# Kernel tuning notes

Measured on AMD Instinct MI355X. Metric: run time of the kernel, lower is better.

## Reference

```python
import jax, jax.numpy as jnp
import numpy as np

FFT_LEN = 512
HOP_LEN = 256
N_BLOCK = 4
N_BIN = FFT_LEN // 2 + 1  # 257
STATE_FACTOR = 0.99999
ALPHA_E = 0.7
BETA_F = 0.1
BATCH = 4096
N_MIC = 1


def setup_inputs() -> dict:
    key = jax.random.key(0)
    ks = jax.random.split(key, 7)
    return {
        "mic": jax.random.normal(ks[0], (BATCH, HOP_LEN, N_MIC), jnp.float32),
        "loudspeaker_buffer": jax.random.normal(ks[1], (BATCH, (N_BLOCK + 1) * HOP_LEN), jnp.float32),
        "phi_e": jax.random.uniform(ks[2], (BATCH, N_BIN, N_MIC), jnp.float32),
        "phi_f": jax.random.uniform(ks[3], (BATCH, N_BIN, N_BLOCK, N_MIC), jnp.float32),
        "P1": jax.random.uniform(ks[4], (BATCH, N_BIN, N_BLOCK, N_MIC), jnp.float32),
        "H_post_real": 0.1 * jax.random.normal(ks[5], (BATCH, N_BIN, N_BLOCK, N_MIC), jnp.float32),
        "H_post_imag": 0.1 * jax.random.normal(ks[6], (BATCH, N_BIN, N_BLOCK, N_MIC), jnp.float32),
    }


def reference(mic, loudspeaker_buffer, phi_e, phi_f, P1, H_post_real, H_post_imag):
    B = mic.shape[0]
    sf2 = STATE_FACTOR * STATE_FACTOR
    H_post = jax.lax.complex(H_post_real, H_post_imag)  # [B, n_bin, n_block, n_mic]

    # STFT of loudspeaker buffer: rectangular window, center=False -> n_block frames
    frame_idx = jnp.arange(N_BLOCK)[:, None] * HOP_LEN + jnp.arange(FFT_LEN)[None, :]
    frames = loudspeaker_buffer[:, frame_idx]              # [B, n_block, fft_len]
    X = jnp.swapaxes(jnp.fft.rfft(frames, axis=-1), 1, 2)  # [B, n_bin, n_block]

    # zero-padded rFFT of mic frame
    zpad = jnp.zeros((B, FFT_LEN - HOP_LEN, N_MIC), mic.dtype)
    fd_mic = jnp.fft.rfft(jnp.concatenate([zpad, mic], axis=1), n=FFT_LEN, axis=1)  # [B, n_bin, n_mic]

    H_prior = H_post
    # a-priori feedback estimate
    fd_fb_hat = jnp.sum(X[..., None] * H_prior, axis=2)                     # [B, n_bin, n_mic]
    est_fb = jnp.fft.irfft(fd_fb_hat, FFT_LEN, axis=1)[:, HOP_LEN:, :]      # [B, hop, n_mic]
    fd_est_fb = jnp.fft.rfft(jnp.concatenate([zpad, est_fb], axis=1), n=FFT_LEN, axis=1)
    E = fd_mic - fd_est_fb                                                  # [B, n_bin, n_mic]

    phi_e = ALPHA_E * phi_e + (1.0 - ALPHA_E) * jnp.abs(E) ** 2

    # Kalman gain
    phi_f = BETA_F * phi_f + (1.0 - BETA_F) * jnp.abs(H_prior) ** 2
    phi_n = (1.0 - sf2) * phi_f
    Xr = jnp.abs(X) ** 2                                                    # [B, n_bin, n_block]
    U = Xr[..., None] * P1                                                  # [B, n_bin, n_block, n_mic]
    R = U + 2.0 * phi_e[:, :, None, :] + 1e-10
    K = P1 * jnp.conj(X)[..., None] / R                                     # [B, n_bin, n_block, n_mic]
    P0 = jax.lax.stop_gradient(P1) - 0.5 * jax.lax.stop_gradient(jnp.abs(K) ** 2 * R)
    P1_new = sf2 * P0 + phi_n  # state update (not part of returned output)

    # filter update via gradient-constrained overlap-save
    dH = jnp.fft.irfft(K * E[:, :, None, :], FFT_LEN, axis=1)               # [B, fft_len, n_block, n_mic]
    mask = (jnp.arange(FFT_LEN) < HOP_LEN).astype(dH.dtype)[None, :, None, None]
    fd_dH = jnp.fft.rfft(dH * mask, n=FFT_LEN, axis=1)                      # [B, n_bin, n_block, n_mic]
    H_post_new = STATE_FACTOR * (H_prior + fd_dH)

    # a-posteriori feedback estimate and enhanced frame
    fd_fb_hat2 = jnp.sum(X[..., None] * H_post_new, axis=2)
    est_fb2 = jnp.fft.irfft(fd_fb_hat2, FFT_LEN, axis=1)[:, HOP_LEN:, :]
    enhanced = mic - est_fb2                                                # [B, hop, n_mic]
    return enhanced
```

## Files before the change

### kernel.cpp

```cpp
#include <hip/hip_runtime.h>
#include <math.h>

#define SF 0.99999f
#define PI2 6.283185307179586476925f
#define SWZ(c) ((c) ^ (((c) >> 4) & 15))
#define LDSFENCE() asm volatile("" ::: "memory")

template<int SGN>
__device__ __forceinline__ void twmul(float& ur, float& ui, float c, float s) {
    const float ss = (SGN < 0) ? -s : s;
    const float r = ur * c - ui * ss;
    const float i = ui * c + ur * ss;
    ur = r; ui = i;
}

template<int SGN>
__device__ __forceinline__ void bfly8(float* ur, float* ui) {
    const float C2 = 0.70710678118654752440f;
    float ar[4], ai[4], br[4], bi[4];
#pragma unroll
    for (int m = 0; m < 4; ++m) {
        ar[m] = ur[m] + ur[m + 4]; ai[m] = ui[m] + ui[m + 4];
        br[m] = ur[m] - ur[m + 4]; bi[m] = ui[m] - ui[m + 4];
    }
    float b1r, b1i, b2r, b2i, b3r, b3i;
    if (SGN < 0) {
        b1r = C2 * (br[1] + bi[1]); b1i = C2 * (bi[1] - br[1]);
        b2r = bi[2];                b2i = -br[2];
        b3r = C2 * (bi[3] - br[3]); b3i = -C2 * (br[3] + bi[3]);
    } else {
        b1r = C2 * (br[1] - bi[1]); b1i = C2 * (bi[1] + br[1]);
        b2r = -bi[2];               b2i = br[2];
        b3r = -C2 * (br[3] + bi[3]); b3i = C2 * (br[3] - bi[3]);
    }
    const float e0r = ar[0] + ar[2], e0i = ai[0] + ai[2];
    const float e1r = ar[0] - ar[2], e1i = ai[0] - ai[2];
    const float o0r = ar[1] + ar[3], o0i = ai[1] + ai[3];
    const float o1r = ar[1] - ar[3], o1i = ai[1] - ai[3];
    ur[0] = e0r + o0r; ui[0] = e0i + o0i;
    ur[4] = e0r - o0r; ui[4] = e0i - o0i;
    if (SGN < 0) { ur[2] = e1r + o1i; ui[2] = e1i - o1r; ur[6] = e1r - o1i; ui[6] = e1i + o1r; }
    else         { ur[2] = e1r - o1i; ui[2] = e1i + o1r; ur[6] = e1r + o1i; ui[6] = e1i - o1r; }
    const float f0r = br[0] + b2r, f0i = bi[0] + b2i;
    const float f1r = br[0] - b2r, f1i = bi[0] - b2i;
    const float g0r = b1r + b3r, g0i = b1i + b3i;
    const float g1r = b1r - b3r, g1i = b1i - b3i;
    ur[1] = f0r + g0r; ui[1] = f0i + g0i;
    ur[5] = f0r - g0r; ui[5] = f0i - g0i;
    if (SGN < 0) { ur[3] = f1r + g1i; ui[3] = f1i - g1r; ur[7] = f1r - g1i; ui[7] = f1i + g1r; }
    else         { ur[3] = f1r - g1i; ui[3] = f1i + g1r; ur[7] = f1r + g1i; ui[7] = f1i - g1r; }
}

template<int SGN>
__device__ __forceinline__ void fft512w(float* ur, float* ui,
                                        float2* __restrict__ buf,
                                        const float2* __restrict__ tw2,
                                        const float2* __restrict__ tw3,
                                        const int* ra, int t) {
    bfly8<SGN>(ur, ui);
    LDSFENCE();
#pragma unroll
    for (int m = 0; m < 8; ++m) buf[SWZ(8 * t + m)] = make_float2(ur[m], ui[m]);
    LDSFENCE();
#pragma unroll
    for (int m = 0; m < 8; ++m) { const float2 v = buf[ra[m]]; ur[m] = v.x; ui[m] = v.y; }
    const int k2 = t & 7;
#pragma unroll
    for (int m = 1; m < 8; ++m) { const float2 w = tw2[m * 8 + k2]; twmul<SGN>(ur[m], ui[m], w.x, w.y); }
    bfly8<SGN>(ur, ui);
    const int jj = ((t >> 3) << 6) + k2;
    LDSFENCE();
#pragma unroll
    for (int m = 0; m < 8; ++m) buf[SWZ(jj + 8 * m)] = make_float2(ur[m], ui[m]);
    LDSFENCE();
#pragma unroll
    for (int m = 0; m < 8; ++m) { const float2 v = buf[ra[m]]; ur[m] = v.x; ui[m] = v.y; }
#pragma unroll
    for (int m = 1; m < 8; ++m) { const float2 w = tw3[m * 64 + t]; twmul<SGN>(ur[m], ui[m], w.x, w.y); }
    bfly8<SGN>(ur, ui);
    LDSFENCE();
}

__global__ __launch_bounds__(64, 2) void pbfd_kernel(
    const float* __restrict__ g_mic,
    const float* __restrict__ g_lsb,
    const float* __restrict__ g_phie,
    const float* __restrict__ g_p1,
    const float* __restrict__ g_hr,
    const float* __restrict__ g_hi,
    float* __restrict__ g_out,
    int B)
{
    __shared__ float2 tw2[64];
    __shared__ float2 tw3[512];
    __shared__ float2 xch[512];

    const int t = threadIdx.x;
    float2* buf = &xch[0];
    const int ml = (64 - t) & 63;

    {
        float s3, c3;
        sincosf(PI2 * (float)t * (1.0f / 512.0f), &s3, &c3);
        float cr = 1.f, ci = 0.f;
#pragma unroll
        for (int m = 0; m < 8; ++m) {
            tw3[m * 64 + t] = make_float2(cr, ci);
            const float nr = cr * c3 - ci * s3;
            ci = ci * c3 + cr * s3;
            cr = nr;
        }
        float s2, c2;
        sincosf(PI2 * (float)((t >> 3) * (t & 7)) * (1.0f / 64.0f), &s2, &c2);
        tw2[t] = make_float2(c2, s2);
    }
    LDSFENCE();

    int ra[8];
#pragma unroll
    for (int m = 0; m < 8; ++m) ra[m] = SWZ(t + 64 * m);

#pragma unroll 1
    for (int ee = 0; ee < 2; ++ee) {
        const int elem = blockIdx.x * 2 + ee;
        if (elem >= B) break;

        float mv[4];
        {
            const float* mp = g_mic + (size_t)elem * 256;
#pragma unroll
            for (int q = 0; q < 4; ++q) mv[q] = mp[t + 64 * q];
        }

        float xr[4][4], xi[4][4], xn[4];
        {
            const float* lb = g_lsb + (size_t)elem * 1280;
#pragma unroll
            for (int pr = 0; pr < 2; ++pr) {
                float ur[8], ui[8];
#pragma unroll
                for (int m = 0; m < 8; ++m) {
                    ur[m] = lb[(2 * pr) * 256 + t + 64 * m];
                    ui[m] = lb[(2 * pr + 1) * 256 + t + 64 * m];
                }
                fft512w<-1>(ur, ui, buf, tw2, tw3, ra, t);
#pragma unroll
                for (int m = 0; m < 4; ++m) {
                    float zmr = __shfl(ur[7 - m], ml);
                    float zmi = __shfl(ui[7 - m], ml);
                    if (t == 0) {
                        zmr = (m == 0) ? ur[0] : ur[8 - m];
                        zmi = (m == 0) ? ui[0] : ui[8 - m];
                    }
                    xr[2 * pr][m]     = 0.5f * (ur[m] + zmr);
                    xi[2 * pr][m]     = 0.5f * (ui[m] - zmi);
                    xr[2 * pr + 1][m] = 0.5f * (ui[m] + zmi);
                    xi[2 * pr + 1][m] = -0.5f * (ur[m] - zmr);
                }
                if (t == 0) { xn[2 * pr] = ur[4]; xn[2 * pr + 1] = ui[4]; }
            }
        }

        auto herm_ifft = [&](const float cr[4], const float ci[4], float cn, float o4[4]) {
            float ur[8], ui[8];
#pragma unroll
            for (int m = 0; m < 4; ++m) { ur[m] = cr[m]; ui[m] = ci[m]; }
#pragma unroll
            for (int m = 4; m < 8; ++m) {
                ur[m] = __shfl(cr[7 - m], ml);
                ui[m] = -__shfl(ci[7 - m], ml);
            }
            if (t == 0) {
                ur[5] = cr[3]; ui[5] = -ci[3];
                ur[6] = cr[2]; ui[6] = -ci[2];
                ur[7] = cr[1]; ui[7] = -ci[1];
                ur[4] = cn; ui[4] = 0.f;
            }
            fft512w<1>(ur, ui, buf, tw2, tw3, ra, t);
#pragma unroll
            for (int q = 0; q < 4; ++q) o4[q] = ur[4 + q] * (1.0f / 512.0f);
        };

        float d4[4];
        float pn[4], en = 0.f, pen = 0.f;
        {
            float cr[4], ci[4], cn = 0.f;
            const float4* hr4 = (const float4*)g_hr + (size_t)elem * 257;
            const float4* hi4 = (const float4*)g_hi + (size_t)elem * 257;
#pragma unroll
            for (int m = 0; m < 4; ++m) {
                const float4 a = hr4[t + 64 * m];
                const float4 b = hi4[t + 64 * m];
                cr[m] = xr[0][m] * a.x - xi[0][m] * b.x + xr[1][m] * a.y - xi[1][m] * b.y
                      + xr[2][m] * a.z - xi[2][m] * b.z + xr[3][m] * a.w - xi[3][m] * b.w;
                ci[m] = xr[0][m] * b.x + xi[0][m] * a.x + xr[1][m] * b.y + xi[1][m] * a.y
                      + xr[2][m] * b.z + xi[2][m] * a.z + xr[3][m] * b.w + xi[3][m] * a.w;
            }
            if (t == 0) {
                const float4 a = hr4[256];
                const float4 p = ((const float4*)g_p1)[(size_t)elem * 257 + 256];
                cn = xn[0] * a.x + xn[1] * a.y + xn[2] * a.z + xn[3] * a.w;
                pn[0] = p.x; pn[1] = p.y; pn[2] = p.z; pn[3] = p.w;
            }
            float o4[4];
            herm_ifft(cr, ci, cn, o4);
#pragma unroll
            for (int q = 0; q < 4; ++q) d4[q] = mv[q] - o4[q];
        }

        float er[4], ei[4];
        {
            float ur[8], ui[8];
#pragma unroll
            for (int m = 0; m < 4; ++m) { ur[m] = 0.f; ui[m] = 0.f; }
#pragma unroll
            for (int q = 0; q < 4; ++q) { ur[4 + q] = d4[q]; ui[4 + q] = 0.f; }
            fft512w<-1>(ur, ui, buf, tw2, tw3, ra, t);
#pragma unroll
            for (int m = 0; m < 4; ++m) { er[m] = ur[m]; ei[m] = ui[m]; }
            if (t == 0) en = ur[4];
        }

        float pe[4];
        {
            const float* php = g_phie + (size_t)elem * 257;
#pragma unroll
            for (int m = 0; m < 4; ++m)
                pe[m] = 0.7f * php[t + 64 * m] + 0.3f * (er[m] * er[m] + ei[m] * ei[m]);
            if (t == 0) pen = 0.7f * php[256] + 0.3f * en * en;
        }

        float Dr[4] = {0, 0, 0, 0}, Di[4] = {0, 0, 0, 0};
        float dn = 0.f;
        {
            const float4* p14 = (const float4*)g_p1 + (size_t)elem * 257;
#pragma unroll
            for (int pr = 0; pr < 2; ++pr) {
                const int j0 = 2 * pr, j1 = 2 * pr + 1;
                float ur[8], ui[8], gr[4], gi[4];
#pragma unroll
                for (int m = 0; m < 4; ++m) {
                    const float4 p = p14[t + 64 * m];
                    const float pa = pr ? p.z : p.x;
                    const float pb = pr ? p.w : p.y;
                    const float xxa = xr[j0][m] * xr[j0][m] + xi[j0][m] * xi[j0][m];
                    const float Ra = xxa * pa + 2.f * pe[m] + 1e-10f;
                    const float ia = 1.f / Ra;
                    const float kra = pa * xr[j0][m] * ia, kia = -pa * xi[j0][m] * ia;
                    const float a_r = kra * er[m] - kia * ei[m];
                    const float a_i = kra * ei[m] + kia * er[m];
                    const float xxb = xr[j1][m] * xr[j1][m] + xi[j1][m] * xi[j1][m];
                    const float Rb = xxb * pb + 2.f * pe[m] + 1e-10f;
                    const float ib = 1.f / Rb;
                    const float krb = pb * xr[j1][m] * ib, kib = -pb * xi[j1][m] * ib;
                    const float b_r = krb * er[m] - kib * ei[m];
                    const float b_i = krb * ei[m] + kib * er[m];
                    ur[m] = a_r - b_i;  ui[m] = a_i + b_r;
                    gr[m] = a_r + b_i;  gi[m] = b_r - a_i;
                }
#pragma unroll
                for (int m = 4; m < 8; ++m) {
                    ur[m] = __shfl(gr[7 - m], ml);
                    ui[m] = __shfl(gi[7 - m], ml);
                }
                if (t == 0) {
                    ur[5] = gr[3]; ui[5] = gi[3];
                    ur[6] = gr[2]; ui[6] = gi[2];
                    ur[7] = gr[1]; ui[7] = gi[1];
                    const float Rn0 = xn[j0] * xn[j0] * pn[j0] + 2.f * pen + 1e-10f;
                    const float Rn1 = xn[j1] * xn[j1] * pn[j1] + 2.f * pen + 1e-10f;
                    ur[4] = pn[j0] * xn[j0] / Rn0 * en;
                    ui[4] = pn[j1] * xn[j1] / Rn1 * en;
                }
                fft512w<1>(ur, ui, buf, tw2, tw3, ra, t);
#pragma unroll
                for (int m = 0; m < 4; ++m) { ur[m] *= (1.0f / 512.0f); ui[m] *= (1.0f / 512.0f); }
#pragma unroll
                for (int m = 4; m < 8; ++m) { ur[m] = 0.f; ui[m] = 0.f; }
                fft512w<-1>(ur, ui, buf, tw2, tw3, ra, t);
#pragma unroll
                for (int m = 0; m < 4; ++m) {
                    float zmr = __shfl(ur[7 - m], ml);
                    float zmi = __shfl(ui[7 - m], ml);
                    if (t == 0) {
                        zmr = (m == 0) ? ur[0] : ur[8 - m];
                        zmi = (m == 0) ? ui[0] : ui[8 - m];
                    }
                    const float f0r = 0.5f * (ur[m] + zmr), f0i = 0.5f * (ui[m] - zmi);
                    const float f1r = 0.5f * (ui[m] + zmi), f1i = -0.5f * (ur[m] - zmr);
                    Dr[m] += xr[j0][m] * f0r - xi[j0][m] * f0i + xr[j1][m] * f1r - xi[j1][m] * f1i;
                    Di[m] += xr[j0][m] * f0i + xi[j0][m] * f0r + xr[j1][m] * f1i + xi[j1][m] * f1r;
                }
                if (t == 0) dn += xn[j0] * ur[4] + xn[j1] * ui[4];
            }
        }

        {
            float o4[4];
            herm_ifft(Dr, Di, dn, o4);
            float* op = g_out + (size_t)elem * 256;
#pragma unroll
            for (int q = 0; q < 4; ++q)
                op[t + 64 * q] = mv[q] - SF * ((mv[q] - d4[q]) + o4[q]);
        }
    }
}

extern "C" void kernel_launch(void* const* d_in, const int* in_sizes, int n_in,
                              void* d_out, int out_size, void* d_ws, size_t ws_size,
                              hipStream_t stream) {
    const float* mic  = (const float*)d_in[0];
    const float* lsb  = (const float*)d_in[1];
    const float* phie = (const float*)d_in[2];
    const float* p1   = (const float*)d_in[4];
    const float* hr   = (const float*)d_in[5];
    const float* hi   = (const float*)d_in[6];
    float* out = (float*)d_out;

    const int B = in_sizes[0] / 256;
    const int blocks = (B + 1) / 2;
    pbfd_kernel<<<blocks, 64, 0, stream>>>(mic, lsb, phie, p1, hr, hi, out, B);
}
```

Before: 37.00 us.

## Keep FFT twiddles in registers, vectorize LDS writes, one element per block

Replaces the shared-memory twiddle tables with per-thread twiddles held in registers, computed once by recurrence. The first FFT transpose now writes to LDS as float4 with a new XOR swizzle, cutting the number of store instructions. The kernel also moves from two batch elements per block to one, so each block is smaller and the grid twice as large. The aim is less LDS traffic and footprint, and so more blocks per CU, at the cost of 32 extra live registers and twice as many twiddle setups overall.

```diff
diff --git a/kernel.cpp b/kernel.cpp
--- a/kernel.cpp
+++ b/kernel.cpp
@@ -54,21 +54,26 @@
 template<int SGN>
 __device__ __forceinline__ void fft512w(float* ur, float* ui,
                                         float2* __restrict__ buf,
-                                        const float2* __restrict__ tw2,
-                                        const float2* __restrict__ tw3,
-                                        const int* ra, int t) {
+                                        const float* t2c, const float* t2s,
+                                        const float* t3c, const float* t3s,
+                                        const int* ra, int wb, int cs, int t) {
     bfly8<SGN>(ur, ui);
     LDSFENCE();
 #pragma unroll
-    for (int m = 0; m < 8; ++m) buf[SWZ(8 * t + m)] = make_float2(ur[m], ui[m]);
+    for (int q = 0; q < 4; ++q) {
+        const int base = wb + ((2 * q) ^ (cs & 6));
+        float4 v;
+        if (cs & 1) v = make_float4(ur[2 * q + 1], ui[2 * q + 1], ur[2 * q], ui[2 * q]);
+        else        v = make_float4(ur[2 * q], ui[2 * q], ur[2 * q + 1], ui[2 * q + 1]);
+        *(float4*)&buf[base] = v;
+    }
     LDSFENCE();
 #pragma unroll
     for (int m = 0; m < 8; ++m) { const float2 v = buf[ra[m]]; ur[m] = v.x; ui[m] = v.y; }
-    const int k2 = t & 7;
-#pragma unroll
-    for (int m = 1; m < 8; ++m) { const float2 w = tw2[m * 8 + k2]; twmul<SGN>(ur[m], ui[m], w.x, w.y); }
+#pragma unroll
+    for (int m = 1; m < 8; ++m) twmul<SGN>(ur[m], ui[m], t2c[m], t2s[m]);
     bfly8<SGN>(ur, ui);
-    const int jj = ((t >> 3) << 6) + k2;
+    const int jj = ((t >> 3) << 6) + (t & 7);
     LDSFENCE();
 #pragma unroll
     for (int m = 0; m < 8; ++m) buf[SWZ(jj + 8 * m)] = make_float2(ur[m], ui[m]);
@@ -76,7 +81,7 @@
 #pragma unroll
     for (int m = 0; m < 8; ++m) { const float2 v = buf[ra[m]]; ur[m] = v.x; ui[m] = v.y; }
 #pragma unroll
-    for (int m = 1; m < 8; ++m) { const float2 w = tw3[m * 64 + t]; twmul<SGN>(ur[m], ui[m], w.x, w.y); }
+    for (int m = 1; m < 8; ++m) twmul<SGN>(ur[m], ui[m], t3c[m], t3s[m]);
     bfly8<SGN>(ur, ui);
     LDSFENCE();
 }
@@ -88,221 +93,216 @@
     const float* __restrict__ g_p1,
     const float* __restrict__ g_hr,
     const float* __restrict__ g_hi,
-    float* __restrict__ g_out,
-    int B)
+    float* __restrict__ g_out)
 {
-    __shared__ float2 tw2[64];
-    __shared__ float2 tw3[512];
-    __shared__ float2 xch[512];
+    __shared__ alignas(16) float2 xch[512];
 
     const int t = threadIdx.x;
+    const int elem = blockIdx.x;
     float2* buf = &xch[0];
     const int ml = (64 - t) & 63;
 
-    {
-        float s3, c3;
+    float t2c[8], t2s[8], t3c[8], t3s[8];
+    {
+        float s2, c2, s3, c3;
+        sincosf(PI2 * (float)(t & 7) * (1.0f / 64.0f), &s2, &c2);
         sincosf(PI2 * (float)t * (1.0f / 512.0f), &s3, &c3);
-        float cr = 1.f, ci = 0.f;
-#pragma unroll
-        for (int m = 0; m < 8; ++m) {
-            tw3[m * 64 + t] = make_float2(cr, ci);
-            const float nr = cr * c3 - ci * s3;
-            ci = ci * c3 + cr * s3;
-            cr = nr;
-        }
-        float s2, c2;
-        sincosf(PI2 * (float)((t >> 3) * (t & 7)) * (1.0f / 64.0f), &s2, &c2);
-        tw2[t] = make_float2(c2, s2);
-    }
-    LDSFENCE();
+        t2c[0] = 1.f; t2s[0] = 0.f; t3c[0] = 1.f; t3s[0] = 0.f;
+        t2c[1] = c2; t2s[1] = s2; t3c[1] = c3; t3s[1] = s3;
+#pragma unroll
+        for (int m = 2; m < 8; ++m) {
+            const float pc2 = t2c[m - 1], ps2 = t2s[m - 1];
+            t2c[m] = pc2 * c2 - ps2 * s2;
+            t2s[m] = ps2 * c2 + pc2 * s2;
+            const float pc3 = t3c[m - 1], ps3 = t3s[m - 1];
+            t3c[m] = pc3 * c3 - ps3 * s3;
+            t3s[m] = ps3 * c3 + pc3 * s3;
+        }
+    }
 
     int ra[8];
 #pragma unroll
     for (int m = 0; m < 8; ++m) ra[m] = SWZ(t + 64 * m);
-
-#pragma unroll 1
-    for (int ee = 0; ee < 2; ++ee) {
-        const int elem = blockIdx.x * 2 + ee;
-        if (elem >= B) break;
-
-        float mv[4];
-        {
-            const float* mp = g_mic + (size_t)elem * 256;
-#pragma unroll
-            for (int q = 0; q < 4; ++q) mv[q] = mp[t + 64 * q];
-        }
-
-        float xr[4][4], xi[4][4], xn[4];
-        {
-            const float* lb = g_lsb + (size_t)elem * 1280;
-#pragma unroll
-            for (int pr = 0; pr < 2; ++pr) {
-                float ur[8], ui[8];
-#pragma unroll
-                for (int m = 0; m < 8; ++m) {
-                    ur[m] = lb[(2 * pr) * 256 + t + 64 * m];
-                    ui[m] = lb[(2 * pr + 1) * 256 + t + 64 * m];
+    const int cs = (t >> 1) & 15;
+    const int wb = (8 * t) ^ (cs & 8);
+
+    float mv[4];
+    {
+        const float* mp = g_mic + (size_t)elem * 256;
+#pragma unroll
+        for (int q = 0; q < 4; ++q) mv[q] = mp[t + 64 * q];
+    }
+
+    float xr[4][4], xi[4][4], xn[4];
+    {
+        const float* lb = g_lsb + (size_t)elem * 1280;
+#pragma unroll
+        for (int pr = 0; pr < 2; ++pr) {
+            float ur[8], ui[8];
+#pragma unroll
+            for (int m = 0; m < 8; ++m) {
+                ur[m] = lb[(2 * pr) * 256 + t + 64 * m];
+                ui[m] = lb[(2 * pr + 1) * 256 + t + 64 * m];
+            }
+            fft512w<-1>(ur, ui, buf, t2c, t2s, t3c, t3s, ra, wb, cs, t);
+#pragma unroll
+            for (int m = 0; m < 4; ++m) {
+                float zmr = __shfl(ur[7 - m], ml);
+                float zmi = __shfl(ui[7 - m], ml);
+                if (t == 0) {
+                    zmr = (m == 0) ? ur[0] : ur[8 - m];
+                    zmi = (m == 0) ? ui[0] : ui[8 - m];
                 }
-                fft512w<-1>(ur, ui, buf, tw2, tw3, ra, t);
-#pragma unroll
-                for (int m = 0; m < 4; ++m) {
-                    float zmr = __shfl(ur[7 - m], ml);
-                    float zmi = __shfl(ui[7 - m], ml);
-                    if (t == 0) {
-                        zmr = (m == 0) ? ur[0] : ur[8 - m];
-                        zmi = (m == 0) ? ui[0] : ui[8 - m];
-                    }
-                    xr[2 * pr][m]     = 0.5f * (ur[m] + zmr);
-                    xi[2 * pr][m]     = 0.5f * (ui[m] - zmi);
-                    xr[2 * pr + 1][m] = 0.5f * (ui[m] + zmi);
-                    xi[2 * pr + 1][m] = -0.5f * (ur[m] - zmr);
+                xr[2 * pr][m]     = 0.5f * (ur[m] + zmr);
+                xi[2 * pr][m]     = 0.5f * (ui[m] - zmi);
+                xr[2 * pr + 1][m] = 0.5f * (ui[m] + zmi);
+                xi[2 * pr + 1][m] = -0.5f * (ur[m] - zmr);
+            }
+            if (t == 0) { xn[2 * pr] = ur[4]; xn[2 * pr + 1] = ui[4]; }
+        }
+    }
+
+    auto herm_ifft = [&](const float cr[4], const float ci[4], float cn, float o4[4]) {
+        float ur[8], ui[8];
+#pragma unroll
+        for (int m = 0; m < 4; ++m) { ur[m] = cr[m]; ui[m] = ci[m]; }
+#pragma unroll
+        for (int m = 4; m < 8; ++m) {
+            ur[m] = __shfl(cr[7 - m], ml);
+            ui[m] = -__shfl(ci[7 - m], ml);
+        }
+        if (t == 0) {
+            ur[5] = cr[3]; ui[5] = -ci[3];
+            ur[6] = cr[2]; ui[6] = -ci[2];
+            ur[7] = cr[1]; ui[7] = -ci[1];
+            ur[4] = cn; ui[4] = 0.f;
+        }
+        fft512w<1>(ur, ui, buf, t2c, t2s, t3c, t3s, ra, wb, cs, t);
+#pragma unroll
+        for (int q = 0; q < 4; ++q) o4[q] = ur[4 + q] * (1.0f / 512.0f);
+    };
+
+    float d4[4];
+    float pn[4], en = 0.f, pen = 0.f;
+    {
+        float cr[4], ci[4], cn = 0.f;
+        const float4* hr4 = (const float4*)g_hr + (size_t)elem * 257;
+        const float4* hi4 = (const float4*)g_hi + (size_t)elem * 257;
+#pragma unroll
+        for (int m = 0; m < 4; ++m) {
+            const float4 a = hr4[t + 64 * m];
+            const float4 b = hi4[t + 64 * m];
+            cr[m] = xr[0][m] * a.x - xi[0][m] * b.x + xr[1][m] * a.y - xi[1][m] * b.y
+                  + xr[2][m] * a.z - xi[2][m] * b.z + xr[3][m] * a.w - xi[3][m] * b.w;
+            ci[m] = xr[0][m] * b.x + xi[0][m] * a.x + xr[1][m] * b.y + xi[1][m] * a.y
+                  + xr[2][m] * b.z + xi[2][m] * a.z + xr[3][m] * b.w + xi[3][m] * a.w;
+        }
+        if (t == 0) {
+            const float4 a = hr4[256];
+            const float4 p = ((const float4*)g_p1)[(size_t)elem * 257 + 256];
+            cn = xn[0] * a.x + xn[1] * a.y + xn[2] * a.z + xn[3] * a.w;
+            pn[0] = p.x; pn[1] = p.y; pn[2] = p.z; pn[3] = p.w;
+        }
+        float o4[4];
+        herm_ifft(cr, ci, cn, o4);
+#pragma unroll
+        for (int q = 0; q < 4; ++q) d4[q] = mv[q] - o4[q];
+    }
+
+    float er[4], ei[4];
+    {
+        float ur[8], ui[8];
+#pragma unroll
+        for (int m = 0; m < 4; ++m) { ur[m] = 0.f; ui[m] = 0.f; }
+#pragma unroll
+        for (int q = 0; q < 4; ++q) { ur[4 + q] = d4[q]; ui[4 + q] = 0.f; }
+        fft512w<-1>(ur, ui, buf, t2c, t2s, t3c, t3s, ra, wb, cs, t);
+#pragma unroll
+        for (int m = 0; m < 4; ++m) { er[m] = ur[m]; ei[m] = ui[m]; }
+        if (t == 0) en = ur[4];
+    }
+
+    float pe[4];
+    {
+        const float* php = g_phie + (size_t)elem * 257;
+#pragma unroll
+        for (int m = 0; m < 4; ++m)
+            pe[m] = 0.7f * php[t + 64 * m] + 0.3f * (er[m] * er[m] + ei[m] * ei[m]);
+        if (t == 0) pen = 0.7f * php[256] + 0.3f * en * en;
+    }
+
+    float Dr[4] = {0, 0, 0, 0}, Di[4] = {0, 0, 0, 0};
+    float dn = 0.f;
+    {
+        const float4* p14 = (const float4*)g_p1 + (size_t)elem * 257;
+#pragma unroll
+        for (int pr = 0; pr < 2; ++pr) {
+            const int j0 = 2 * pr, j1 = 2 * pr + 1;
+            float ur[8], ui[8], gr[4], gi[4];
+#pragma unroll
+            for (int m = 0; m < 4; ++m) {
+                const float4 p = p14[t + 64 * m];
+                const float pa = pr ? p.z : p.x;
+                const float pb = pr ? p.w : p.y;
+                const float xxa = xr[j0][m] * xr[j0][m] + xi[j0][m] * xi[j0][m];
+                const float Ra = xxa * pa + 2.f * pe[m] + 1e-10f;
+                const float ia = 1.f / Ra;
+                const float kra = pa * xr[j0][m] * ia, kia = -pa * xi[j0][m] * ia;
+                const float a_r = kra * er[m] - kia * ei[m];
+                const float a_i = kra * ei[m] + kia * er[m];
+                const float xxb = xr[j1][m] * xr[j1][m] + xi[j1][m] * xi[j1][m];
+                const float Rb = xxb * pb + 2.f * pe[m] + 1e-10f;
+                const float ib = 1.f / Rb;
+                const float krb = pb * xr[j1][m] * ib, kib = -pb * xi[j1][m] * ib;
+                const float b_r = krb * er[m] - kib * ei[m];
+                const float b_i = krb * ei[m] + kib * er[m];
+                ur[m] = a_r - b_i;  ui[m] = a_i + b_r;
+                gr[m] = a_r + b_i;  gi[m] = b_r - a_i;
+            }
+#pragma unroll
+            for (int m = 4; m < 8; ++m) {
+                ur[m] = __shfl(gr[7 - m], ml);
+                ui[m] = __shfl(gi[7 - m], ml);
+            }
+            if (t == 0) {
+                ur[5] = gr[3]; ui[5] = gi[3];
+                ur[6] = gr[2]; ui[6] = gi[2];
+                ur[7] = gr[1]; ui[7] = gi[1];
+                const float Rn0 = xn[j0] * xn[j0] * pn[j0] + 2.f * pen + 1e-10f;
+                const float Rn1 = xn[j1] * xn[j1] * pn[j1] + 2.f * pen + 1e-10f;
+                ur[4] = pn[j0] * xn[j0] / Rn0 * en;
+                ui[4] = pn[j1] * xn[j1] / Rn1 * en;
+            }
+            fft512w<1>(ur, ui, buf, t2c, t2s, t3c, t3s, ra, wb, cs, t);
+#pragma unroll
+            for (int m = 0; m < 4; ++m) { ur[m] *= (1.0f / 512.0f); ui[m] *= (1.0f / 512.0f); }
+#pragma unroll
+            for (int m = 4; m < 8; ++m) { ur[m] = 0.f; ui[m] = 0.f; }
+            fft512w<-1>(ur, ui, buf, t2c, t2s, t3c, t3s, ra, wb, cs, t);
+#pragma unroll
+            for (int m = 0; m < 4; ++m) {
+                float zmr = __shfl(ur[7 - m], ml);
+                float zmi = __shfl(ui[7 - m], ml);
+                if (t == 0) {
+                    zmr = (m == 0) ? ur[0] : ur[8 - m];
+                    zmi = (m == 0) ? ui[0] : ui[8 - m];
                 }
-                if (t == 0) { xn[2 * pr] = ur[4]; xn[2 * pr + 1] = ui[4]; }
-            }
-        }
-
-        auto herm_ifft = [&](const float cr[4], const float ci[4], float cn, float o4[4]) {
-            float ur[8], ui[8];
-#pragma unroll
-            for (int m = 0; m < 4; ++m) { ur[m] = cr[m]; ui[m] = ci[m]; }
-#pragma unroll
-            for (int m = 4; m < 8; ++m) {
-                ur[m] = __shfl(cr[7 - m], ml);
-                ui[m] = -__shfl(ci[7 - m], ml);
-            }
-            if (t == 0) {
-                ur[5] = cr[3]; ui[5] = -ci[3];
-                ur[6] = cr[2]; ui[6] = -ci[2];
-                ur[7] = cr[1]; ui[7] = -ci[1];
-                ur[4] = cn; ui[4] = 0.f;
-            }
-            fft512w<1>(ur, ui, buf, tw2, tw3, ra, t);
-#pragma unroll
-            for (int q = 0; q < 4; ++q) o4[q] = ur[4 + q] * (1.0f / 512.0f);
-        };
-
-        float d4[4];
-        float pn[4], en = 0.f, pen = 0.f;
-        {
-            float cr[4], ci[4], cn = 0.f;
-            const float4* hr4 = (const float4*)g_hr + (size_t)elem * 257;
-            const float4* hi4 = (const float4*)g_hi + (size_t)elem * 257;
-#pragma unroll
-            for (int m = 0; m < 4; ++m) {
-                const float4 a = hr4[t + 64 * m];
-                const float4 b = hi4[t + 64 * m];
-                cr[m] = xr[0][m] * a.x - xi[0][m] * b.x + xr[1][m] * a.y - xi[1][m] * b.y
-                      + xr[2][m] * a.z - xi[2][m] * b.z + xr[3][m] * a.w - xi[3][m] * b.w;
-                ci[m] = xr[0][m] * b.x + xi[0][m] * a.x + xr[1][m] * b.y + xi[1][m] * a.y
-                      + xr[2][m] * b.z + xi[2][m] * a.z + xr[3][m] * b.w + xi[3][m] * a.w;
-            }
-            if (t == 0) {
-                const float4 a = hr4[256];
-                const float4 p = ((const float4*)g_p1)[(size_t)elem * 257 + 256];
-                cn = xn[0] * a.x + xn[1] * a.y + xn[2] * a.z + xn[3] * a.w;
-                pn[0] = p.x; pn[1] = p.y; pn[2] = p.z; pn[3] = p.w;
-            }
-            float o4[4];
-            herm_ifft(cr, ci, cn, o4);
-#pragma unroll
-            for (int q = 0; q < 4; ++q) d4[q] = mv[q] - o4[q];
-        }
-
-        float er[4], ei[4];
-        {
-            float ur[8], ui[8];
-#pragma unroll
-            for (int m = 0; m < 4; ++m) { ur[m] = 0.f; ui[m] = 0.f; }
-#pragma unroll
-            for (int q = 0; q < 4; ++q) { ur[4 + q] = d4[q]; ui[4 + q] = 0.f; }
-            fft512w<-1>(ur, ui, buf, tw2, tw3, ra, t);
-#pragma unroll
-            for (int m = 0; m < 4; ++m) { er[m] = ur[m]; ei[m] = ui[m]; }
-            if (t == 0) en = ur[4];
-        }
-
-        float pe[4];
-        {
-            const float* php = g_phie + (size_t)elem * 257;
-#pragma unroll
-            for (int m = 0; m < 4; ++m)
-                pe[m] = 0.7f * php[t + 64 * m] + 0.3f * (er[m] * er[m] + ei[m] * ei[m]);
-            if (t == 0) pen = 0.7f * php[256] + 0.3f * en * en;
-        }
-
-        float Dr[4] = {0, 0, 0, 0}, Di[4] = {0, 0, 0, 0};
-        float dn = 0.f;
-        {
-            const float4* p14 = (const float4*)g_p1 + (size_t)elem * 257;
-#pragma unroll
-            for (int pr = 0; pr < 2; ++pr) {
-                const int j0 = 2 * pr, j1 = 2 * pr + 1;
-                float ur[8], ui[8], gr[4], gi[4];
-#pragma unroll
-                for (int m = 0; m < 4; ++m) {
-                    const float4 p = p14[t + 64 * m];
-                    const float pa = pr ? p.z : p.x;
-                    const float pb = pr ? p.w : p.y;
-                    const float xxa = xr[j0][m] * xr[j0][m] + xi[j0][m] * xi[j0][m];
-                    const float Ra = xxa * pa + 2.f * pe[m] + 1e-10f;
-                    const float ia = 1.f / Ra;
-                    const float kra = pa * xr[j0][m] * ia, kia = -pa * xi[j0][m] * ia;
-                    const float a_r = kra * er[m] - kia * ei[m];
-                    const float a_i = kra * ei[m] + kia * er[m];
-                    const float xxb = xr[j1][m] * xr[j1][m] + xi[j1][m] * xi[j1][m];
-                    const float Rb = xxb * pb + 2.f * pe[m] + 1e-10f;
-                    const float ib = 1.f / Rb;
-                    const float krb = pb * xr[j1][m] * ib, kib = -pb * xi[j1][m] * ib;
-                    const float b_r = krb * er[m] - kib * ei[m];
-                    const float b_i = krb * ei[m] + kib * er[m];
-                    ur[m] = a_r - b_i;  ui[m] = a_i + b_r;
-                    gr[m] = a_r + b_i;  gi[m] = b_r - a_i;
-                }
-#pragma unroll
-                for (int m = 4; m < 8; ++m) {
-                    ur[m] = __shfl(gr[7 - m], ml);
-                    ui[m] = __shfl(gi[7 - m], ml);
-                }
-                if (t == 0) {
-                    ur[5] = gr[3]; ui[5] = gi[3];
-                    ur[6] = gr[2]; ui[6] = gi[2];
-                    ur[7] = gr[1]; ui[7] = gi[1];
-                    const float Rn0 = xn[j0] * xn[j0] * pn[j0] + 2.f * pen + 1e-10f;
-                    const float Rn1 = xn[j1] * xn[j1] * pn[j1] + 2.f * pen + 1e-10f;
-                    ur[4] = pn[j0] * xn[j0] / Rn0 * en;
-                    ui[4] = pn[j1] * xn[j1] / Rn1 * en;
-                }
-                fft512w<1>(ur, ui, buf, tw2, tw3, ra, t);
-#pragma unroll
-                for (int m = 0; m < 4; ++m) { ur[m] *= (1.0f / 512.0f); ui[m] *= (1.0f / 512.0f); }
-#pragma unroll
-                for (int m = 4; m < 8; ++m) { ur[m] = 0.f; ui[m] = 0.f; }
-                fft512w<-1>(ur, ui, buf, tw2, tw3, ra, t);
-#pragma unroll
-                for (int m = 0; m < 4; ++m) {
-                    float zmr = __shfl(ur[7 - m], ml);
-                    float zmi = __shfl(ui[7 - m], ml);
-                    if (t == 0) {
-                        zmr = (m == 0) ? ur[0] : ur[8 - m];
-                        zmi = (m == 0) ? ui[0] : ui[8 - m];
-                    }
-                    const float f0r = 0.5f * (ur[m] + zmr), f0i = 0.5f * (ui[m] - zmi);
-                    const float f1r = 0.5f * (ui[m] + zmi), f1i = -0.5f * (ur[m] - zmr);
-                    Dr[m] += xr[j0][m] * f0r - xi[j0][m] * f0i + xr[j1][m] * f1r - xi[j1][m] * f1i;
-                    Di[m] += xr[j0][m] * f0i + xi[j0][m] * f0r + xr[j1][m] * f1i + xi[j1][m] * f1r;
-                }
-                if (t == 0) dn += xn[j0] * ur[4] + xn[j1] * ui[4];
-            }
-        }
-
-        {
-            float o4[4];
-            herm_ifft(Dr, Di, dn, o4);
-            float* op = g_out + (size_t)elem * 256;
-#pragma unroll
-            for (int q = 0; q < 4; ++q)
-                op[t + 64 * q] = mv[q] - SF * ((mv[q] - d4[q]) + o4[q]);
-        }
+                const float f0r = 0.5f * (ur[m] + zmr), f0i = 0.5f * (ui[m] - zmi);
+                const float f1r = 0.5f * (ui[m] + zmi), f1i = -0.5f * (ur[m] - zmr);
+                Dr[m] += xr[j0][m] * f0r - xi[j0][m] * f0i + xr[j1][m] * f1r - xi[j1][m] * f1i;
+                Di[m] += xr[j0][m] * f0i + xi[j0][m] * f0r + xr[j1][m] * f1i + xi[j1][m] * f1r;
+            }
+            if (t == 0) dn += xn[j0] * ur[4] + xn[j1] * ui[4];
+        }
+    }
+
+    {
+        float o4[4];
+        herm_ifft(Dr, Di, dn, o4);
+        float* op = g_out + (size_t)elem * 256;
+#pragma unroll
+        for (int q = 0; q < 4; ++q)
+            op[t + 64 * q] = mv[q] - SF * ((mv[q] - d4[q]) + o4[q]);
     }
 }
 
@@ -318,6 +318,5 @@
     float* out = (float*)d_out;
 
     const int B = in_sizes[0] / 256;
-    const int blocks = (B + 1) / 2;
-    pbfd_kernel<<<blocks, 64, 0, stream>>>(mic, lsb, phie, p1, hr, hi, out, B);
-}
+    pbfd_kernel<<<B, 64, 0, stream>>>(mic, lsb, phie, p1, hr, hi, out);
+}
```

New measurement: 53.55 us. 44.7% more time.
